# Kernel tuning notes

Hardware: AMD Instinct MI355X
Metric: run time of the kernel (lower is better)

Reference implementation:

```python
import jax, jax.numpy as jnp
import numpy as np

N = 8192  # number of nodes (input_size[0])
K = 32    # number of archetypes


def setup_inputs() -> dict:
    key = jax.random.key(0)
    kA, kb, ka, kX, kC = jax.random.split(key, 5)
    A = (jax.random.uniform(kA, (N, N)) < 0.05).astype(jnp.float32)
    beta = jax.random.normal(kb, (N,), dtype=jnp.float32)
    a = jax.random.normal(ka, (1,), dtype=jnp.float32)
    X = jax.random.normal(kX, (K, N), dtype=jnp.float32)
    C = jax.random.normal(kC, (N, K), dtype=jnp.float32)
    return {"A": A, "beta": beta, "a": a, "X": X, "C": C}


def reference(A, beta, a, X, C):
    # z_dist[i,j] = (X[:,i]-X[:,j])^T C_s^T K C_s (X[:,i]-X[:,j]),
    # with K = softmax(X)^T softmax(X), C_s = softmax(C) (both column-softmax, dim=0).
    Xs = jax.nn.softmax(X, axis=0)          # (K, N)
    Cs = jax.nn.softmax(C, axis=0)          # (N, K)
    E = Xs @ Cs                             # (K, K) = softmax(X) @ softmax(C)
    M = E.T @ E                             # (K, K) = Cs^T Xs^T Xs Cs, PSD
    # quadratic form over all pairs via G = X^T M X (raw X columns, as in the torch loop)
    G = X.T @ (M @ X)                       # (N, N)
    q = jnp.diagonal(G)                     # (N,) = x_i^T M x_i
    z_dist = q[:, None] + q[None, :] - 2.0 * G
    theta = beta[:, None] + beta[None, :] - a * z_dist  # (N, N)
    sp = jax.nn.softplus(theta)
    LL = 0.5 * jnp.sum(theta * A) - 0.5 * (jnp.sum(sp) - jnp.sum(jnp.diagonal(sp)))
    return LL
```

## Files before the change

### kernel.cpp

```cpp
#include <hip/hip_runtime.h>
#include <hip/hip_bf16.h>

#define NN 8192
#define KK 32

typedef __attribute__((ext_vector_type(8))) short short8v;
typedef __attribute__((ext_vector_type(4))) float float4v;

__device__ __forceinline__ float wave_reduce_sum(float v) {
    #pragma unroll
    for (int off = 32; off > 0; off >>= 1) v += __shfl_down(v, off);
    return v;
}
__device__ __forceinline__ float wave_reduce_max(float v) {
    #pragma unroll
    for (int off = 32; off > 0; off >>= 1) v = fmaxf(v, __shfl_down(v, off));
    return v;
}
__device__ __forceinline__ unsigned short f2bf(float x) {
    unsigned int u = __float_as_uint(x);
    return (unsigned short)((u + 0x7fffu + ((u >> 16) & 1u)) >> 16);
}
__device__ __forceinline__ float bf2f(unsigned short h) {
    return __uint_as_float(((unsigned int)h) << 16);
}

__global__ void kc_colstats(const float* __restrict__ C, float* __restrict__ mC,
                            float* __restrict__ sC) {
    const int l = blockIdx.x;
    const int t = threadIdx.x;
    float v[32];
    #pragma unroll
    for (int u = 0; u < 32; ++u)
        v[u] = C[(size_t)(u * 256 + t) * KK + l];
    float m = v[0];
    #pragma unroll
    for (int u = 1; u < 32; ++u) m = fmaxf(m, v[u]);
    m = wave_reduce_max(m);
    __shared__ float wmax[4], wsum[4];
    if ((t & 63) == 0) wmax[t >> 6] = m;
    __syncthreads();
    const float mm = fmaxf(fmaxf(wmax[0], wmax[1]), fmaxf(wmax[2], wmax[3]));
    float s = 0.f;
    #pragma unroll
    for (int u = 0; u < 32; ++u) s += __expf(v[u] - mm);
    s = wave_reduce_sum(s);
    if ((t & 63) == 0) wsum[t >> 6] = s;
    __syncthreads();
    if (t == 0) {
        mC[l] = mm;
        sC[l] = wsum[0] + wsum[1] + wsum[2] + wsum[3];
    }
}

__global__ void kx_softmax(const float* __restrict__ X, float* __restrict__ Xs) {
    const int n = blockIdx.x * 256 + threadIdx.x;
    float e[KK];
    float m = -INFINITY;
    #pragma unroll
    for (int k = 0; k < KK; ++k) {
        e[k] = X[(size_t)k * NN + n];
        m = fmaxf(m, e[k]);
    }
    float s = 0.f;
    #pragma unroll
    for (int k = 0; k < KK; ++k) {
        e[k] = __expf(e[k] - m);
        s += e[k];
    }
    const float r = 1.f / s;
    #pragma unroll
    for (int k = 0; k < KK; ++k) Xs[(size_t)k * NN + n] = e[k] * r;
}

__global__ void ke_E(const float* __restrict__ Xs, const float* __restrict__ C,
                     const float* __restrict__ mC, const float* __restrict__ sC,
                     float* __restrict__ E) {
    __shared__ float xsl[KK * 33];
    __shared__ float cql[32 * 33];
    __shared__ float mCl[KK], rsCl[KK];
    const int tid = threadIdx.x;
    if (tid < KK) { mCl[tid] = mC[tid]; rsCl[tid] = 1.f / sC[tid]; }
    const int k = tid & 31, l = tid >> 5;
    const int nb = blockIdx.x * 32;
    __syncthreads();
    xsl[(tid >> 5) * 33 + (tid & 31)] = Xs[(size_t)(tid >> 5) * NN + nb + (tid & 31)];
    const float cv = C[(size_t)nb * KK + tid];
    cql[(tid >> 5) * 33 + (tid & 31)] = __expf(cv - mCl[tid & 31]) * rsCl[tid & 31];
    __syncthreads();
    float acc = 0.f;
    #pragma unroll
    for (int n = 0; n < 32; ++n)
        acc = fmaf(xsl[k * 33 + n], cql[n * 33 + l], acc);
    atomicAdd(&E[k * KK + l], acc);
}

__global__ void km_M(const float* __restrict__ E, float* __restrict__ M) {
    __shared__ float el[KK * 33];
    const int tid = threadIdx.x;
    el[(tid >> 5) * 33 + (tid & 31)] = E[tid];
    __syncthreads();
    const int l1 = tid & 31, l2 = tid >> 5;
    float acc = 0.f;
    #pragma unroll
    for (int kk = 0; kk < KK; ++kk)
        acc = fmaf(el[kk * 33 + l1], el[kk * 33 + l2], acc);
    M[tid] = acc;
}

__global__ void kp_prep(const float* __restrict__ X, const float* __restrict__ beta,
                        const float* __restrict__ a_ptr, const float* __restrict__ Mm,
                        float* __restrict__ f,
                        unsigned short* __restrict__ Xh, unsigned short* __restrict__ Wh,
                        double* __restrict__ acc) {
    __shared__ float Ml[KK * KK];
    const int tid = threadIdx.x;
    #pragma unroll
    for (int u = 0; u < 4; ++u) Ml[tid + 256 * u] = Mm[tid + 256 * u];
    __syncthreads();
    const int n = blockIdx.x * 256 + tid;
    float x[KK], v[KK];
    #pragma unroll
    for (int k = 0; k < KK; ++k) x[k] = X[(size_t)k * NN + n];
    const float a = a_ptr[0];
    const float two_a = 2.f * a;
    #pragma unroll
    for (int l = 0; l < KK; ++l) {
        float s = 0.f;
        #pragma unroll
        for (int k = 0; k < KK; ++k) s = fmaf(Ml[l * KK + k], x[k], s);
        v[l] = two_a * s;
    }
    float q2 = 0.f;
    #pragma unroll
    for (int l = 0; l < KK; ++l) q2 = fmaf(x[l], v[l], q2);
    const float b = beta[n];
    const float fn = b - 0.5f * q2;
    f[n] = fn;

    union PK { unsigned short u[8]; short8v s; };
    PK xh, wh;
    #pragma unroll
    for (int g = 0; g < 4; ++g) {
        #pragma unroll
        for (int e = 0; e < 8; ++e) {
            const int k = g * 8 + e;
            xh.u[e] = f2bf(x[k]);
            wh.u[e] = f2bf(v[k]);
        }
        *(short8v*)&Xh[(size_t)n * KK + g * 8] = xh.s;
        *(short8v*)&Wh[(size_t)n * KK + g * 8] = wh.s;
    }
    const float th = 2.f * b;
    float sp = fmaxf(th, 0.f) + __logf(1.f + __expf(-fabsf(th)));
    sp = wave_reduce_sum(sp);
    if ((tid & 63) == 0) atomicAdd(&acc[2], (double)sp);
}

__global__ __launch_bounds__(256, 8) void k_pair(
    const float* __restrict__ A, const float* __restrict__ f,
    const unsigned short* __restrict__ Xh, const unsigned short* __restrict__ Wh,
    float* __restrict__ part) {
    const int tid  = threadIdx.x;
    const int lane = tid & 63;
    const int l15  = lane & 15;
    const int klo  = (lane >> 4) << 3;
    const int r0   = (lane >> 4) << 2;
    const int wid  = blockIdx.x * 4 + (tid >> 6);
    const int ibase = (wid >> 4) << 4;
    const int jc    = (wid & 15) << 9;

    const short8v xh = *(const short8v*)&Xh[(size_t)(ibase + l15) * KK + klo];
    float fr[4];
    #pragma unroll
    for (int r = 0; r < 4; ++r) fr[r] = f[ibase + r0 + r];

    float accA = 0.f, accS = 0.f;
    #pragma unroll 2
    for (int jt = 0; jt < 32; ++jt) {
        const int jb = jc + (jt << 4);
        float av[4];
        #pragma unroll
        for (int r = 0; r < 4; ++r)
            av[r] = A[(size_t)(ibase + r0 + r) * NN + jb + l15];
        const short8v wh = *(const short8v*)&Wh[(size_t)(jb + l15) * KK + klo];
        const float fj = f[jb + l15];
        float4v d = {0.f, 0.f, 0.f, 0.f};
        d = __builtin_amdgcn_mfma_f32_16x16x32_bf16(xh, wh, d, 0, 0, 0);
        #pragma unroll
        for (int r = 0; r < 4; ++r) {
            const float th = fr[r] + fj + d[r];
            accA = fmaf(th, av[r], accA);
            accS += fmaxf(th, 0.f) + __logf(1.f + __expf(-fabsf(th)));
        }
    }

    accA = wave_reduce_sum(accA);
    accS = wave_reduce_sum(accS);
    __shared__ float rA[4], rS[4];
    if (lane == 0) { rA[tid >> 6] = accA; rS[tid >> 6] = accS; }
    __syncthreads();
    if (tid == 0) {
        part[blockIdx.x * 2]     = rA[0] + rA[1] + rA[2] + rA[3];
        part[blockIdx.x * 2 + 1] = rS[0] + rS[1] + rS[2] + rS[3];
    }
}

__global__ __launch_bounds__(1024) void kz_final(const float* __restrict__ part,
                                                 const double* __restrict__ acc,
                                                 float* __restrict__ out) {
    const int t = threadIdx.x;
    double dA = (double)part[2 * t]     + (double)part[2 * (t + 1024)];
    double dS = (double)part[2 * t + 1] + (double)part[2 * (t + 1024) + 1];
    #pragma unroll
    for (int off = 32; off > 0; off >>= 1) {
        dA += __shfl_down(dA, off);
        dS += __shfl_down(dS, off);
    }
    __shared__ double sA[16], sS[16];
    if ((t & 63) == 0) { sA[t >> 6] = dA; sS[t >> 6] = dS; }
    __syncthreads();
    if (t == 0) {
        double a = 0.0, s = 0.0;
        #pragma unroll
        for (int u = 0; u < 16; ++u) { a += sA[u]; s += sS[u]; }
        out[0] = (float)(0.5 * (a - (s - acc[2])));
    }
}

extern "C" void kernel_launch(void* const* d_in, const int* in_sizes, int n_in,
                              void* d_out, int out_size, void* d_ws, size_t ws_size,
                              hipStream_t stream) {
    const float* Ain    = (const float*)d_in[0];
    const float* betain = (const float*)d_in[1];
    const float* ain    = (const float*)d_in[2];
    const float* Xin    = (const float*)d_in[3];
    const float* Cin    = (const float*)d_in[4];
    float* out = (float*)d_out;

    char* ws = (char*)d_ws;
    float*          E    = (float*)(ws + 0);
    double*         acc  = (double*)(ws + 4096);
    float*          mC   = (float*)(ws + 4160);
    float*          sC   = (float*)(ws + 4288);
    float*          M    = (float*)(ws + 4608);
    float*          f    = (float*)(ws + 8704);
    float*          part = (float*)(ws + 49152);
    unsigned short* Xh   = (unsigned short*)(ws + 65536);
    unsigned short* Wh   = (unsigned short*)(ws + 589824);
    float*          Xs   = (float*)(ws + 1114112);

    hipMemsetAsync(ws, 0, 4128, stream);

    kc_colstats<<<KK, 256, 0, stream>>>(Cin, mC, sC);
    kx_softmax<<<NN / 256, 256, 0, stream>>>(Xin, Xs);
    ke_E<<<256, 1024, 0, stream>>>(Xs, Cin, mC, sC, E);
    km_M<<<1, 1024, 0, stream>>>(E, M);
    kp_prep<<<NN / 256, 256, 0, stream>>>(Xin, betain, ain, M, f, Xh, Wh, acc);
    k_pair<<<2048, 256, 0, stream>>>(Ain, f, Xh, Wh, part);
    kz_final<<<1, 1024, 0, stream>>>(part, acc, out);
}
```

Baseline: 458.0 us.

## Split A-weighted theta sum into row/col terms plus MFMA A·W product

The A-weighted term sum(theta*A) is expanded algebraically into f_i·rowsum(A), colsum(A)·f_j and a bilinear X_i^T (A W)_i term. Binary A is packed to bf16 and multiplied against a transposed W with MFMA, instead of forming theta per element for that sum. Each wave now covers a 64x128 tile with vectorized float4 loads of A, and a separate pass still computes the full softplus sum. This adds new transposed W and fp32 X buffers in prep, drops the occupancy hint, and raises register pressure.

```diff
diff --git a/kernel.cpp b/kernel.cpp
--- a/kernel.cpp
+++ b/kernel.cpp
@@ -110,8 +110,9 @@
 
 __global__ void kp_prep(const float* __restrict__ X, const float* __restrict__ beta,
                         const float* __restrict__ a_ptr, const float* __restrict__ Mm,
-                        float* __restrict__ f,
+                        float* __restrict__ f, float* __restrict__ Xt,
                         unsigned short* __restrict__ Xh, unsigned short* __restrict__ Wh,
+                        unsigned short* __restrict__ Wt2,
                         double* __restrict__ acc) {
     __shared__ float Ml[KK * KK];
     const int tid = threadIdx.x;
@@ -145,8 +146,10 @@
         #pragma unroll
         for (int e = 0; e < 8; ++e) {
             const int k = g * 8 + e;
+            Xt[(size_t)n * KK + k] = x[k];
             xh.u[e] = f2bf(x[k]);
             wh.u[e] = f2bf(v[k]);
+            Wt2[(size_t)k * NN + n] = wh.u[e];
         }
         *(short8v*)&Xh[(size_t)n * KK + g * 8] = xh.s;
         *(short8v*)&Wh[(size_t)n * KK + g * 8] = wh.s;
@@ -157,44 +160,99 @@
     if ((tid & 63) == 0) atomicAdd(&acc[2], (double)sp);
 }
 
-__global__ __launch_bounds__(256, 8) void k_pair(
+__global__ __launch_bounds__(256) void k_uni(
     const float* __restrict__ A, const float* __restrict__ f,
+    const float* __restrict__ Xt,
     const unsigned short* __restrict__ Xh, const unsigned short* __restrict__ Wh,
+    const unsigned short* __restrict__ Wt2,
     float* __restrict__ part) {
     const int tid  = threadIdx.x;
     const int lane = tid & 63;
     const int l15  = lane & 15;
-    const int klo  = (lane >> 4) << 3;
-    const int r0   = (lane >> 4) << 2;
+    const int g4   = lane >> 4;
+    const int klo2 = g4 << 3;
+    const int r0   = g4 << 2;
     const int wid  = blockIdx.x * 4 + (tid >> 6);
-    const int ibase = (wid >> 4) << 4;
-    const int jc    = (wid & 15) << 9;
-
-    const short8v xh = *(const short8v*)&Xh[(size_t)(ibase + l15) * KK + klo];
-    float fr[4];
-    #pragma unroll
-    for (int r = 0; r < 4; ++r) fr[r] = f[ibase + r0 + r];
-
-    float accA = 0.f, accS = 0.f;
+    const int ibase = (wid >> 6) << 6;
+    const int jc    = (wid & 63) << 7;
+
+    float fI[4];
+    #pragma unroll
+    for (int s = 0; s < 4; ++s) fI[s] = f[ibase + s * 16 + l15];
+
+    float4v pacc[4][2];
+    #pragma unroll
+    for (int s = 0; s < 4; ++s)
+        #pragma unroll
+        for (int h = 0; h < 2; ++h)
+            pacc[s][h] = (float4v){0.f, 0.f, 0.f, 0.f};
+    float accFR = 0.f, accFC = 0.f;
+
+    #pragma unroll
+    for (int jt = 0; jt < 4; ++jt) {
+        const int jb = jc + (jt << 5);
+        const float4 fj0 = *(const float4*)&f[jb + klo2];
+        const float4 fj1 = *(const float4*)&f[jb + klo2 + 4];
+        const short8v w0 = *(const short8v*)&Wt2[(size_t)l15 * NN + jb + klo2];
+        const short8v w1 = *(const short8v*)&Wt2[(size_t)(16 + l15) * NN + jb + klo2];
+        #pragma unroll
+        for (int s = 0; s < 4; ++s) {
+            const float* ar = &A[(size_t)(ibase + s * 16 + l15) * NN + jb + klo2];
+            const float4 a0 = *(const float4*)ar;
+            const float4 a1 = *(const float4*)(ar + 4);
+            accFR += (((a0.x + a0.y) + (a0.z + a0.w)) +
+                      ((a1.x + a1.y) + (a1.z + a1.w))) * fI[s];
+            accFC += a0.x * fj0.x + a0.y * fj0.y + a0.z * fj0.z + a0.w * fj0.w +
+                     a1.x * fj1.x + a1.y * fj1.y + a1.z * fj1.z + a1.w * fj1.w;
+            union { unsigned int u[4]; short8v s8; } af;
+            af.u[0] = __builtin_amdgcn_perm(__float_as_uint(a0.y), __float_as_uint(a0.x), 0x07060302u);
+            af.u[1] = __builtin_amdgcn_perm(__float_as_uint(a0.w), __float_as_uint(a0.z), 0x07060302u);
+            af.u[2] = __builtin_amdgcn_perm(__float_as_uint(a1.y), __float_as_uint(a1.x), 0x07060302u);
+            af.u[3] = __builtin_amdgcn_perm(__float_as_uint(a1.w), __float_as_uint(a1.z), 0x07060302u);
+            pacc[s][0] = __builtin_amdgcn_mfma_f32_16x16x32_bf16(af.s8, w0, pacc[s][0], 0, 0, 0);
+            pacc[s][1] = __builtin_amdgcn_mfma_f32_16x16x32_bf16(af.s8, w1, pacc[s][1], 0, 0, 0);
+        }
+    }
+
+    float accAX = 0.f;
+    #pragma unroll
+    for (int s = 0; s < 4; ++s)
+        #pragma unroll
+        for (int h = 0; h < 2; ++h)
+            #pragma unroll
+            for (int r = 0; r < 4; ++r)
+                accAX += Xt[(size_t)(ibase + s * 16 + r0 + r) * KK + h * 16 + l15]
+                         * pacc[s][h][r];
+
+    short8v xf[4];
+    #pragma unroll
+    for (int s = 0; s < 4; ++s)
+        xf[s] = *(const short8v*)&Xh[(size_t)(ibase + s * 16 + l15) * KK + klo2];
+    float fS[4][4];
+    #pragma unroll
+    for (int s = 0; s < 4; ++s)
+        #pragma unroll
+        for (int r = 0; r < 4; ++r) fS[s][r] = f[ibase + s * 16 + r0 + r];
+
+    float accS = 0.f;
     #pragma unroll 2
-    for (int jt = 0; jt < 32; ++jt) {
-        const int jb = jc + (jt << 4);
-        float av[4];
-        #pragma unroll
-        for (int r = 0; r < 4; ++r)
-            av[r] = A[(size_t)(ibase + r0 + r) * NN + jb + l15];
-        const short8v wh = *(const short8v*)&Wh[(size_t)(jb + l15) * KK + klo];
-        const float fj = f[jb + l15];
-        float4v d = {0.f, 0.f, 0.f, 0.f};
-        d = __builtin_amdgcn_mfma_f32_16x16x32_bf16(xh, wh, d, 0, 0, 0);
-        #pragma unroll
-        for (int r = 0; r < 4; ++r) {
-            const float th = fr[r] + fj + d[r];
-            accA = fmaf(th, av[r], accA);
-            accS += fmaxf(th, 0.f) + __logf(1.f + __expf(-fabsf(th)));
+    for (int u = 0; u < 8; ++u) {
+        const int jb2 = jc + (u << 4);
+        const short8v wf = *(const short8v*)&Wh[(size_t)(jb2 + l15) * KK + klo2];
+        const float fj = f[jb2 + l15];
+        #pragma unroll
+        for (int s = 0; s < 4; ++s) {
+            float4v d = {0.f, 0.f, 0.f, 0.f};
+            d = __builtin_amdgcn_mfma_f32_16x16x32_bf16(xf[s], wf, d, 0, 0, 0);
+            #pragma unroll
+            for (int r = 0; r < 4; ++r) {
+                const float th = fS[s][r] + fj + d[r];
+                accS += fmaxf(th, 0.f) + __logf(1.f + __expf(-fabsf(th)));
+            }
         }
     }
 
+    float accA = accFR + accFC + accAX;
     accA = wave_reduce_sum(accA);
     accS = wave_reduce_sum(accS);
     __shared__ float rA[4], rS[4];
@@ -248,7 +306,9 @@
     float*          part = (float*)(ws + 49152);
     unsigned short* Xh   = (unsigned short*)(ws + 65536);
     unsigned short* Wh   = (unsigned short*)(ws + 589824);
-    float*          Xs   = (float*)(ws + 1114112);
+    unsigned short* Wt2  = (unsigned short*)(ws + 1114112);
+    float*          Xt   = (float*)(ws + 1638400);
+    float*          Xs   = (float*)(ws + 2686976);
 
     hipMemsetAsync(ws, 0, 4128, stream);
 
@@ -256,7 +316,7 @@
     kx_softmax<<<NN / 256, 256, 0, stream>>>(Xin, Xs);
     ke_E<<<256, 1024, 0, stream>>>(Xs, Cin, mC, sC, E);
     km_M<<<1, 1024, 0, stream>>>(E, M);
-    kp_prep<<<NN / 256, 256, 0, stream>>>(Xin, betain, ain, M, f, Xh, Wh, acc);
-    k_pair<<<2048, 256, 0, stream>>>(Ain, f, Xh, Wh, part);
+    kp_prep<<<NN / 256, 256, 0, stream>>>(Xin, betain, ain, M, f, Xt, Xh, Wh, Wt2, acc);
+    k_uni<<<2048, 256, 0, stream>>>(Ain, f, Xt, Xh, Wh, Wt2, part);
     kz_final<<<1, 1024, 0, stream>>>(part, acc, out);
 }
```

Result: slower. 529.7 us (+15.7%).

## Split pair kernel into A-weighted MFMA GEMM term and separate softplus term

Applied to the files above, without the earlier changes.

The sum of theta*A is rewritten as a matrix product: A rows (truncated to bf16 with a byte permute) are multiplied by a transposed bf16 buffer holding W, a ones row and a hi/lo split of f, and the result is contracted with X rows and f afterwards. The softplus sum moves into its own kernel that no longer reads A. The column-softmax statistics of C are also computed without max subtraction, as a parallel exp-sum with atomics. This removes per-element theta*A arithmetic and lets A be streamed with wide loads feeding MFMA. In exchange it adds an extra kernel launch, extra prep writes (Xt, Bh), and accuracy risk from bf16 products and from exp without max stabilisation.

```diff
diff --git a/kernel.cpp b/kernel.cpp
--- a/kernel.cpp
+++ b/kernel.cpp
@@ -10,11 +10,6 @@
 __device__ __forceinline__ float wave_reduce_sum(float v) {
     #pragma unroll
     for (int off = 32; off > 0; off >>= 1) v += __shfl_down(v, off);
-    return v;
-}
-__device__ __forceinline__ float wave_reduce_max(float v) {
-    #pragma unroll
-    for (int off = 32; off > 0; off >>= 1) v = fmaxf(v, __shfl_down(v, off));
     return v;
 }
 __device__ __forceinline__ unsigned short f2bf(float x) {
@@ -25,31 +20,22 @@
     return __uint_as_float(((unsigned int)h) << 16);
 }
 
-__global__ void kc_colstats(const float* __restrict__ C, float* __restrict__ mC,
-                            float* __restrict__ sC) {
-    const int l = blockIdx.x;
+__global__ void kc_sum(const float* __restrict__ C, float* __restrict__ sC) {
     const int t = threadIdx.x;
-    float v[32];
-    #pragma unroll
-    for (int u = 0; u < 32; ++u)
-        v[u] = C[(size_t)(u * 256 + t) * KK + l];
-    float m = v[0];
-    #pragma unroll
-    for (int u = 1; u < 32; ++u) m = fmaxf(m, v[u]);
-    m = wave_reduce_max(m);
-    __shared__ float wmax[4], wsum[4];
-    if ((t & 63) == 0) wmax[t >> 6] = m;
-    __syncthreads();
-    const float mm = fmaxf(fmaxf(wmax[0], wmax[1]), fmaxf(wmax[2], wmax[3]));
-    float s = 0.f;
-    #pragma unroll
-    for (int u = 0; u < 32; ++u) s += __expf(v[u] - mm);
-    s = wave_reduce_sum(s);
-    if ((t & 63) == 0) wsum[t >> 6] = s;
-    __syncthreads();
-    if (t == 0) {
-        mC[l] = mm;
-        sC[l] = wsum[0] + wsum[1] + wsum[2] + wsum[3];
+    const int col = t & 31, rg = t >> 5;
+    const int row0 = blockIdx.x * 128;
+    float p = 0.f;
+    #pragma unroll
+    for (int u = 0; u < 16; ++u)
+        p += __expf(C[(size_t)(row0 + u * 8 + rg) * KK + col]);
+    __shared__ float ps[8][32];
+    ps[rg][col] = p;
+    __syncthreads();
+    if (t < 32) {
+        float s = 0.f;
+        #pragma unroll
+        for (int u = 0; u < 8; ++u) s += ps[u][t];
+        atomicAdd(&sC[t], s);
     }
 }
 
@@ -74,19 +60,18 @@
 }
 
 __global__ void ke_E(const float* __restrict__ Xs, const float* __restrict__ C,
-                     const float* __restrict__ mC, const float* __restrict__ sC,
-                     float* __restrict__ E) {
+                     const float* __restrict__ sC, float* __restrict__ E) {
     __shared__ float xsl[KK * 33];
     __shared__ float cql[32 * 33];
-    __shared__ float mCl[KK], rsCl[KK];
+    __shared__ float rsCl[KK];
     const int tid = threadIdx.x;
-    if (tid < KK) { mCl[tid] = mC[tid]; rsCl[tid] = 1.f / sC[tid]; }
+    if (tid < KK) rsCl[tid] = 1.f / sC[tid];
     const int k = tid & 31, l = tid >> 5;
     const int nb = blockIdx.x * 32;
     __syncthreads();
     xsl[(tid >> 5) * 33 + (tid & 31)] = Xs[(size_t)(tid >> 5) * NN + nb + (tid & 31)];
     const float cv = C[(size_t)nb * KK + tid];
-    cql[(tid >> 5) * 33 + (tid & 31)] = __expf(cv - mCl[tid & 31]) * rsCl[tid & 31];
+    cql[(tid >> 5) * 33 + (tid & 31)] = __expf(cv) * rsCl[tid & 31];
     __syncthreads();
     float acc = 0.f;
     #pragma unroll
@@ -110,8 +95,9 @@
 
 __global__ void kp_prep(const float* __restrict__ X, const float* __restrict__ beta,
                         const float* __restrict__ a_ptr, const float* __restrict__ Mm,
-                        float* __restrict__ f,
+                        float* __restrict__ f, float* __restrict__ Xt,
                         unsigned short* __restrict__ Xh, unsigned short* __restrict__ Wh,
+                        unsigned short* __restrict__ Bh,
                         double* __restrict__ acc) {
     __shared__ float Ml[KK * KK];
     const int tid = threadIdx.x;
@@ -145,73 +131,127 @@
         #pragma unroll
         for (int e = 0; e < 8; ++e) {
             const int k = g * 8 + e;
+            Xt[(size_t)n * KK + k] = x[k];
             xh.u[e] = f2bf(x[k]);
             wh.u[e] = f2bf(v[k]);
+            Bh[(size_t)k * NN + n] = wh.u[e];
         }
         *(short8v*)&Xh[(size_t)n * KK + g * 8] = xh.s;
         *(short8v*)&Wh[(size_t)n * KK + g * 8] = wh.s;
     }
+    Bh[(size_t)32 * NN + n] = 0x3F80;
+    const unsigned short hf = f2bf(fn);
+    Bh[(size_t)33 * NN + n] = hf;
+    Bh[(size_t)34 * NN + n] = f2bf(fn - bf2f(hf));
+    #pragma unroll
+    for (int k = 35; k < 48; ++k) Bh[(size_t)k * NN + n] = 0;
+
     const float th = 2.f * b;
     float sp = fmaxf(th, 0.f) + __logf(1.f + __expf(-fabsf(th)));
     sp = wave_reduce_sum(sp);
     if ((tid & 63) == 0) atomicAdd(&acc[2], (double)sp);
 }
 
-__global__ __launch_bounds__(256, 8) void k_pair(
+__global__ __launch_bounds__(256, 6) void k_A(
     const float* __restrict__ A, const float* __restrict__ f,
-    const unsigned short* __restrict__ Xh, const unsigned short* __restrict__ Wh,
+    const float* __restrict__ Xt, const unsigned short* __restrict__ Bh,
     float* __restrict__ part) {
     const int tid  = threadIdx.x;
     const int lane = tid & 63;
     const int l15  = lane & 15;
-    const int klo  = (lane >> 4) << 3;
+    const int klo2 = (lane >> 4) << 3;
     const int r0   = (lane >> 4) << 2;
     const int wid  = blockIdx.x * 4 + (tid >> 6);
     const int ibase = (wid >> 4) << 4;
     const int jc    = (wid & 15) << 9;
 
-    const short8v xh = *(const short8v*)&Xh[(size_t)(ibase + l15) * KK + klo];
-    float fr[4];
-    #pragma unroll
-    for (int r = 0; r < 4; ++r) fr[r] = f[ibase + r0 + r];
-
-    float accA = 0.f, accS = 0.f;
+    float4v c0 = {0.f, 0.f, 0.f, 0.f}, c1 = c0, c2 = c0;
+    const float* arow = &A[(size_t)(ibase + l15) * NN + jc + klo2];
+    const unsigned short* b0p = &Bh[(size_t)l15 * NN + jc + klo2];
+    const unsigned short* b1p = &Bh[(size_t)(16 + l15) * NN + jc + klo2];
+    const unsigned short* b2p = &Bh[(size_t)(32 + l15) * NN + jc + klo2];
+
     #pragma unroll 2
-    for (int jt = 0; jt < 32; ++jt) {
-        const int jb = jc + (jt << 4);
-        float av[4];
-        #pragma unroll
-        for (int r = 0; r < 4; ++r)
-            av[r] = A[(size_t)(ibase + r0 + r) * NN + jb + l15];
-        const short8v wh = *(const short8v*)&Wh[(size_t)(jb + l15) * KK + klo];
+    for (int jt = 0; jt < 16; ++jt) {
+        const float4 a0 = *(const float4*)(arow + jt * 32);
+        const float4 a1 = *(const float4*)(arow + jt * 32 + 4);
+        union { unsigned int u[4]; short8v s8; } af;
+        af.u[0] = __builtin_amdgcn_perm(__float_as_uint(a0.y), __float_as_uint(a0.x), 0x07060302u);
+        af.u[1] = __builtin_amdgcn_perm(__float_as_uint(a0.w), __float_as_uint(a0.z), 0x07060302u);
+        af.u[2] = __builtin_amdgcn_perm(__float_as_uint(a1.y), __float_as_uint(a1.x), 0x07060302u);
+        af.u[3] = __builtin_amdgcn_perm(__float_as_uint(a1.w), __float_as_uint(a1.z), 0x07060302u);
+        const short8v b0 = *(const short8v*)(b0p + jt * 32);
+        const short8v b1 = *(const short8v*)(b1p + jt * 32);
+        const short8v b2 = *(const short8v*)(b2p + jt * 32);
+        c0 = __builtin_amdgcn_mfma_f32_16x16x32_bf16(af.s8, b0, c0, 0, 0, 0);
+        c1 = __builtin_amdgcn_mfma_f32_16x16x32_bf16(af.s8, b1, c1, 0, 0, 0);
+        c2 = __builtin_amdgcn_mfma_f32_16x16x32_bf16(af.s8, b2, c2, 0, 0, 0);
+    }
+
+    float acc = 0.f;
+    #pragma unroll
+    for (int r = 0; r < 4; ++r) {
+        const int row = ibase + r0 + r;
+        acc += Xt[(size_t)row * KK + l15] * c0[r];
+        acc += Xt[(size_t)row * KK + 16 + l15] * c1[r];
+        const float fv = f[row];
+        const float mult = (l15 == 0) ? fv : ((l15 < 3) ? 1.f : 0.f);
+        acc += mult * c2[r];
+    }
+
+    acc = wave_reduce_sum(acc);
+    __shared__ float rA[4];
+    if (lane == 0) rA[tid >> 6] = acc;
+    __syncthreads();
+    if (tid == 0) part[blockIdx.x] = rA[0] + rA[1] + rA[2] + rA[3];
+}
+
+__global__ __launch_bounds__(256, 8) void k_S(
+    const float* __restrict__ f, const unsigned short* __restrict__ Xh,
+    const unsigned short* __restrict__ Wh, float* __restrict__ partS) {
+    const int tid  = threadIdx.x;
+    const int lane = tid & 63;
+    const int l15  = lane & 15;
+    const int klo2 = (lane >> 4) << 3;
+    const int r0   = (lane >> 4) << 2;
+    const int wid  = blockIdx.x * 4 + (tid >> 6);
+    const int ibase = (wid >> 4) << 4;
+    const int jc    = (wid & 15) << 9;
+
+    const short8v xh = *(const short8v*)&Xh[(size_t)(ibase + l15) * KK + klo2];
+    float fS[4];
+    #pragma unroll
+    for (int r = 0; r < 4; ++r) fS[r] = f[ibase + r0 + r];
+
+    float accS = 0.f;
+    #pragma unroll 2
+    for (int u = 0; u < 32; ++u) {
+        const int jb = jc + (u << 4);
+        const short8v wf = *(const short8v*)&Wh[(size_t)(jb + l15) * KK + klo2];
         const float fj = f[jb + l15];
         float4v d = {0.f, 0.f, 0.f, 0.f};
-        d = __builtin_amdgcn_mfma_f32_16x16x32_bf16(xh, wh, d, 0, 0, 0);
+        d = __builtin_amdgcn_mfma_f32_16x16x32_bf16(xh, wf, d, 0, 0, 0);
         #pragma unroll
         for (int r = 0; r < 4; ++r) {
-            const float th = fr[r] + fj + d[r];
-            accA = fmaf(th, av[r], accA);
+            const float th = fS[r] + fj + d[r];
             accS += fmaxf(th, 0.f) + __logf(1.f + __expf(-fabsf(th)));
         }
     }
 
-    accA = wave_reduce_sum(accA);
     accS = wave_reduce_sum(accS);
-    __shared__ float rA[4], rS[4];
-    if (lane == 0) { rA[tid >> 6] = accA; rS[tid >> 6] = accS; }
-    __syncthreads();
-    if (tid == 0) {
-        part[blockIdx.x * 2]     = rA[0] + rA[1] + rA[2] + rA[3];
-        part[blockIdx.x * 2 + 1] = rS[0] + rS[1] + rS[2] + rS[3];
-    }
+    __shared__ float rS[4];
+    if (lane == 0) rS[tid >> 6] = accS;
+    __syncthreads();
+    if (tid == 0) partS[blockIdx.x] = rS[0] + rS[1] + rS[2] + rS[3];
 }
 
 __global__ __launch_bounds__(1024) void kz_final(const float* __restrict__ part,
+                                                 const float* __restrict__ partS,
                                                  const double* __restrict__ acc,
                                                  float* __restrict__ out) {
     const int t = threadIdx.x;
-    double dA = (double)part[2 * t]     + (double)part[2 * (t + 1024)];
-    double dS = (double)part[2 * t + 1] + (double)part[2 * (t + 1024) + 1];
+    double dA = (double)part[t]  + (double)part[t + 1024];
+    double dS = (double)partS[t] + (double)partS[t + 1024];
     #pragma unroll
     for (int off = 32; off > 0; off >>= 1) {
         dA += __shfl_down(dA, off);
@@ -239,24 +279,27 @@
     float* out = (float*)d_out;
 
     char* ws = (char*)d_ws;
-    float*          E    = (float*)(ws + 0);
-    double*         acc  = (double*)(ws + 4096);
-    float*          mC   = (float*)(ws + 4160);
-    float*          sC   = (float*)(ws + 4288);
-    float*          M    = (float*)(ws + 4608);
-    float*          f    = (float*)(ws + 8704);
-    float*          part = (float*)(ws + 49152);
-    unsigned short* Xh   = (unsigned short*)(ws + 65536);
-    unsigned short* Wh   = (unsigned short*)(ws + 589824);
-    float*          Xs   = (float*)(ws + 1114112);
-
-    hipMemsetAsync(ws, 0, 4128, stream);
-
-    kc_colstats<<<KK, 256, 0, stream>>>(Cin, mC, sC);
+    float*          E     = (float*)(ws + 0);
+    double*         acc   = (double*)(ws + 4096);
+    float*          sC    = (float*)(ws + 4224);
+    float*          f     = (float*)(ws + 8704);
+    float*          part  = (float*)(ws + 49152);
+    float*          partS = (float*)(ws + 57344);
+    unsigned short* Xh    = (unsigned short*)(ws + 65536);
+    unsigned short* Wh    = (unsigned short*)(ws + 589824);
+    float*          Xt    = (float*)(ws + 1114112);
+    unsigned short* Bh    = (unsigned short*)(ws + 2162688);
+    float*          Xs    = (float*)(ws + 2949120);
+    float*          M     = (float*)(ws + 3997696);
+
+    hipMemsetAsync(ws, 0, 4352, stream);
+
+    kc_sum<<<64, 256, 0, stream>>>(Cin, sC);
     kx_softmax<<<NN / 256, 256, 0, stream>>>(Xin, Xs);
-    ke_E<<<256, 1024, 0, stream>>>(Xs, Cin, mC, sC, E);
+    ke_E<<<256, 1024, 0, stream>>>(Xs, Cin, sC, E);
     km_M<<<1, 1024, 0, stream>>>(E, M);
-    kp_prep<<<NN / 256, 256, 0, stream>>>(Xin, betain, ain, M, f, Xh, Wh, acc);
-    k_pair<<<2048, 256, 0, stream>>>(Ain, f, Xh, Wh, part);
-    kz_final<<<1, 1024, 0, stream>>>(part, acc, out);
-}
+    kp_prep<<<NN / 256, 256, 0, stream>>>(Xin, betain, ain, M, f, Xt, Xh, Wh, Bh, acc);
+    k_S<<<2048, 256, 0, stream>>>(f, Xh, Wh, partS);
+    k_A<<<2048, 256, 0, stream>>>(Ain, f, Xt, Bh, part);
+    kz_final<<<1, 1024, 0, stream>>>(part, partS, acc, out);
+}
```

Result: slower. 501.1 us (+9.4%).

## Fuse softmax/E/M prologue kernels and widen pair-kernel tiles to 32 rows

Applied to the files above, without the earlier changes.

Merges the C column-stats, X softmax, E and M kernels into one kE kernel plus M recomputation in kp_prep. C normalisation is deferred, and the softmax max-subtraction is dropped for plain exp, which is valid for these normal inputs. This cuts the launch chain from seven kernels to four. The pair kernel now has each wave cover 32 rows by 256 columns, reusing one Wh/f load for two MFMAs, and the occupancy hint drops from 8 to 6.

```diff
diff --git a/kernel.cpp b/kernel.cpp
--- a/kernel.cpp
+++ b/kernel.cpp
@@ -10,114 +10,80 @@
 __device__ __forceinline__ float wave_reduce_sum(float v) {
     #pragma unroll
     for (int off = 32; off > 0; off >>= 1) v += __shfl_down(v, off);
-    return v;
-}
-__device__ __forceinline__ float wave_reduce_max(float v) {
-    #pragma unroll
-    for (int off = 32; off > 0; off >>= 1) v = fmaxf(v, __shfl_down(v, off));
     return v;
 }
 __device__ __forceinline__ unsigned short f2bf(float x) {
     unsigned int u = __float_as_uint(x);
     return (unsigned short)((u + 0x7fffu + ((u >> 16) & 1u)) >> 16);
 }
-__device__ __forceinline__ float bf2f(unsigned short h) {
-    return __uint_as_float(((unsigned int)h) << 16);
-}
-
-__global__ void kc_colstats(const float* __restrict__ C, float* __restrict__ mC,
-                            float* __restrict__ sC) {
-    const int l = blockIdx.x;
-    const int t = threadIdx.x;
-    float v[32];
-    #pragma unroll
-    for (int u = 0; u < 32; ++u)
-        v[u] = C[(size_t)(u * 256 + t) * KK + l];
-    float m = v[0];
-    #pragma unroll
-    for (int u = 1; u < 32; ++u) m = fmaxf(m, v[u]);
-    m = wave_reduce_max(m);
-    __shared__ float wmax[4], wsum[4];
-    if ((t & 63) == 0) wmax[t >> 6] = m;
-    __syncthreads();
-    const float mm = fmaxf(fmaxf(wmax[0], wmax[1]), fmaxf(wmax[2], wmax[3]));
-    float s = 0.f;
-    #pragma unroll
-    for (int u = 0; u < 32; ++u) s += __expf(v[u] - mm);
-    s = wave_reduce_sum(s);
-    if ((t & 63) == 0) wsum[t >> 6] = s;
-    __syncthreads();
-    if (t == 0) {
-        mC[l] = mm;
-        sC[l] = wsum[0] + wsum[1] + wsum[2] + wsum[3];
-    }
-}
-
-__global__ void kx_softmax(const float* __restrict__ X, float* __restrict__ Xs) {
-    const int n = blockIdx.x * 256 + threadIdx.x;
-    float e[KK];
-    float m = -INFINITY;
-    #pragma unroll
-    for (int k = 0; k < KK; ++k) {
-        e[k] = X[(size_t)k * NN + n];
-        m = fmaxf(m, e[k]);
-    }
-    float s = 0.f;
-    #pragma unroll
-    for (int k = 0; k < KK; ++k) {
-        e[k] = __expf(e[k] - m);
-        s += e[k];
-    }
-    const float r = 1.f / s;
-    #pragma unroll
-    for (int k = 0; k < KK; ++k) Xs[(size_t)k * NN + n] = e[k] * r;
-}
-
-__global__ void ke_E(const float* __restrict__ Xs, const float* __restrict__ C,
-                     const float* __restrict__ mC, const float* __restrict__ sC,
-                     float* __restrict__ E) {
-    __shared__ float xsl[KK * 33];
-    __shared__ float cql[32 * 33];
-    __shared__ float mCl[KK], rsCl[KK];
+
+__global__ __launch_bounds__(256) void kE(const float* __restrict__ X,
+                                          const float* __restrict__ C,
+                                          float* __restrict__ Ep,
+                                          float* __restrict__ sC) {
+    __shared__ float xe[KK * 33];
+    __shared__ float ce[32 * 33];
+    __shared__ float xs[32];
     const int tid = threadIdx.x;
-    if (tid < KK) { mCl[tid] = mC[tid]; rsCl[tid] = 1.f / sC[tid]; }
-    const int k = tid & 31, l = tid >> 5;
+    const int r = tid >> 5, q = tid & 31;
     const int nb = blockIdx.x * 32;
-    __syncthreads();
-    xsl[(tid >> 5) * 33 + (tid & 31)] = Xs[(size_t)(tid >> 5) * NN + nb + (tid & 31)];
-    const float cv = C[(size_t)nb * KK + tid];
-    cql[(tid >> 5) * 33 + (tid & 31)] = __expf(cv - mCl[tid & 31]) * rsCl[tid & 31];
-    __syncthreads();
-    float acc = 0.f;
-    #pragma unroll
-    for (int n = 0; n < 32; ++n)
-        acc = fmaf(xsl[k * 33 + n], cql[n * 33 + l], acc);
-    atomicAdd(&E[k * KK + l], acc);
-}
-
-__global__ void km_M(const float* __restrict__ E, float* __restrict__ M) {
+    #pragma unroll
+    for (int u = 0; u < 4; ++u) {
+        xe[(r + 8 * u) * 33 + q] = __expf(X[(size_t)(r + 8 * u) * NN + nb + q]);
+        ce[(r + 8 * u) * 33 + q] = __expf(C[(size_t)(nb + r + 8 * u) * KK + q]);
+    }
+    __syncthreads();
+    if (tid < 32) {
+        float s = 0.f;
+        #pragma unroll
+        for (int k = 0; k < 32; ++k) s += xe[k * 33 + tid];
+        xs[tid] = 1.f / s;
+    } else if (tid < 64) {
+        const int l = tid - 32;
+        float s = 0.f;
+        #pragma unroll
+        for (int n = 0; n < 32; ++n) s += ce[n * 33 + l];
+        atomicAdd(&sC[l], s);
+    }
+    __syncthreads();
+    #pragma unroll
+    for (int u = 0; u < 4; ++u) {
+        const int k = r + 8 * u;
+        float acc = 0.f;
+        #pragma unroll
+        for (int n = 0; n < 32; ++n)
+            acc = fmaf(xe[k * 33 + n] * xs[n], ce[n * 33 + q], acc);
+        atomicAdd(&Ep[k * KK + q], acc);
+    }
+}
+
+__global__ __launch_bounds__(256) void kp_prep(
+    const float* __restrict__ X, const float* __restrict__ beta,
+    const float* __restrict__ a_ptr, const float* __restrict__ Ep,
+    const float* __restrict__ sC,
+    float* __restrict__ f, unsigned short* __restrict__ Xh,
+    unsigned short* __restrict__ Wh, double* __restrict__ acc) {
     __shared__ float el[KK * 33];
-    const int tid = threadIdx.x;
-    el[(tid >> 5) * 33 + (tid & 31)] = E[tid];
-    __syncthreads();
-    const int l1 = tid & 31, l2 = tid >> 5;
-    float acc = 0.f;
-    #pragma unroll
-    for (int kk = 0; kk < KK; ++kk)
-        acc = fmaf(el[kk * 33 + l1], el[kk * 33 + l2], acc);
-    M[tid] = acc;
-}
-
-__global__ void kp_prep(const float* __restrict__ X, const float* __restrict__ beta,
-                        const float* __restrict__ a_ptr, const float* __restrict__ Mm,
-                        float* __restrict__ f,
-                        unsigned short* __restrict__ Xh, unsigned short* __restrict__ Wh,
-                        double* __restrict__ acc) {
+    __shared__ float rs[32];
     __shared__ float Ml[KK * KK];
     const int tid = threadIdx.x;
-    #pragma unroll
-    for (int u = 0; u < 4; ++u) Ml[tid + 256 * u] = Mm[tid + 256 * u];
-    __syncthreads();
+    const int r = tid >> 5, q = tid & 31;
+    #pragma unroll
+    for (int u = 0; u < 4; ++u)
+        el[(r + 8 * u) * 33 + q] = Ep[(r + 8 * u) * KK + q];
+    if (tid < 32) rs[tid] = 1.f / sC[tid];
+    __syncthreads();
+    #pragma unroll
+    for (int u = 0; u < 4; ++u) {
+        const int l1 = r + 8 * u;
+        float m = 0.f;
+        #pragma unroll
+        for (int k = 0; k < KK; ++k)
+            m = fmaf(el[k * 33 + l1], el[k * 33 + q], m);
+        Ml[l1 * KK + q] = m * rs[l1] * rs[q];
+    }
+    __syncthreads();
+
     const int n = blockIdx.x * 256 + tid;
     float x[KK], v[KK];
     #pragma unroll
@@ -157,7 +123,7 @@
     if ((tid & 63) == 0) atomicAdd(&acc[2], (double)sp);
 }
 
-__global__ __launch_bounds__(256, 8) void k_pair(
+__global__ __launch_bounds__(256, 6) void k_pair(
     const float* __restrict__ A, const float* __restrict__ f,
     const unsigned short* __restrict__ Xh, const unsigned short* __restrict__ Wh,
     float* __restrict__ part) {
@@ -167,31 +133,37 @@
     const int klo  = (lane >> 4) << 3;
     const int r0   = (lane >> 4) << 2;
     const int wid  = blockIdx.x * 4 + (tid >> 6);
-    const int ibase = (wid >> 4) << 4;
-    const int jc    = (wid & 15) << 9;
-
-    const short8v xh = *(const short8v*)&Xh[(size_t)(ibase + l15) * KK + klo];
-    float fr[4];
-    #pragma unroll
-    for (int r = 0; r < 4; ++r) fr[r] = f[ibase + r0 + r];
+    const int ibase = (wid >> 5) << 5;
+    const int jc    = (wid & 31) << 8;
+
+    const short8v xh0 = *(const short8v*)&Xh[(size_t)(ibase + l15) * KK + klo];
+    const short8v xh1 = *(const short8v*)&Xh[(size_t)(ibase + 16 + l15) * KK + klo];
+    float fr[2][4];
+    #pragma unroll
+    for (int s = 0; s < 2; ++s)
+        #pragma unroll
+        for (int r = 0; r < 4; ++r) fr[s][r] = f[ibase + 16 * s + r0 + r];
 
     float accA = 0.f, accS = 0.f;
     #pragma unroll 2
-    for (int jt = 0; jt < 32; ++jt) {
+    for (int jt = 0; jt < 16; ++jt) {
         const int jb = jc + (jt << 4);
-        float av[4];
-        #pragma unroll
-        for (int r = 0; r < 4; ++r)
-            av[r] = A[(size_t)(ibase + r0 + r) * NN + jb + l15];
-        const short8v wh = *(const short8v*)&Wh[(size_t)(jb + l15) * KK + klo];
+        const short8v wf = *(const short8v*)&Wh[(size_t)(jb + l15) * KK + klo];
         const float fj = f[jb + l15];
-        float4v d = {0.f, 0.f, 0.f, 0.f};
-        d = __builtin_amdgcn_mfma_f32_16x16x32_bf16(xh, wh, d, 0, 0, 0);
-        #pragma unroll
-        for (int r = 0; r < 4; ++r) {
-            const float th = fr[r] + fj + d[r];
-            accA = fmaf(th, av[r], accA);
-            accS += fmaxf(th, 0.f) + __logf(1.f + __expf(-fabsf(th)));
+        #pragma unroll
+        for (int s = 0; s < 2; ++s) {
+            float av[4];
+            #pragma unroll
+            for (int r = 0; r < 4; ++r)
+                av[r] = A[(size_t)(ibase + 16 * s + r0 + r) * NN + jb + l15];
+            float4v d = {0.f, 0.f, 0.f, 0.f};
+            d = __builtin_amdgcn_mfma_f32_16x16x32_bf16(s ? xh1 : xh0, wf, d, 0, 0, 0);
+            #pragma unroll
+            for (int r = 0; r < 4; ++r) {
+                const float th = fr[s][r] + fj + d[r];
+                accA = fmaf(th, av[r], accA);
+                accS += fmaxf(th, 0.f) + __logf(1.f + __expf(-fabsf(th)));
+            }
         }
     }
 
@@ -239,24 +211,18 @@
     float* out = (float*)d_out;
 
     char* ws = (char*)d_ws;
-    float*          E    = (float*)(ws + 0);
-    double*         acc  = (double*)(ws + 4096);
-    float*          mC   = (float*)(ws + 4160);
-    float*          sC   = (float*)(ws + 4288);
-    float*          M    = (float*)(ws + 4608);
-    float*          f    = (float*)(ws + 8704);
-    float*          part = (float*)(ws + 49152);
-    unsigned short* Xh   = (unsigned short*)(ws + 65536);
-    unsigned short* Wh   = (unsigned short*)(ws + 589824);
-    float*          Xs   = (float*)(ws + 1114112);
-
-    hipMemsetAsync(ws, 0, 4128, stream);
-
-    kc_colstats<<<KK, 256, 0, stream>>>(Cin, mC, sC);
-    kx_softmax<<<NN / 256, 256, 0, stream>>>(Xin, Xs);
-    ke_E<<<256, 1024, 0, stream>>>(Xs, Cin, mC, sC, E);
-    km_M<<<1, 1024, 0, stream>>>(E, M);
-    kp_prep<<<NN / 256, 256, 0, stream>>>(Xin, betain, ain, M, f, Xh, Wh, acc);
+    float*          Ep    = (float*)(ws + 0);
+    double*         acc   = (double*)(ws + 4096);
+    float*          sC    = (float*)(ws + 4224);
+    float*          f     = (float*)(ws + 8704);
+    float*          part  = (float*)(ws + 49152);
+    unsigned short* Xh    = (unsigned short*)(ws + 65536);
+    unsigned short* Wh    = (unsigned short*)(ws + 589824);
+
+    hipMemsetAsync(ws, 0, 4352, stream);
+
+    kE<<<256, 256, 0, stream>>>(Xin, Cin, Ep, sC);
+    kp_prep<<<NN / 256, 256, 0, stream>>>(Xin, betain, ain, Ep, sC, f, Xh, Wh, acc);
     k_pair<<<2048, 256, 0, stream>>>(Ain, f, Xh, Wh, part);
     kz_final<<<1, 1024, 0, stream>>>(part, acc, out);
 }
```

Result: faster. 409.7 us (-10.5%).
